# Performance work log

Measured on AMD Instinct MI355X. Metric: run time of the kernel, lower is better.

## Reference

```python
import jax, jax.numpy as jnp
import numpy as np

NUM_GROUPS = 32
EPS = 1e-5


def group_norm(x, weight, bias):
    # x: [B, C, N]
    B, C, N = x.shape
    g = x.reshape(B, NUM_GROUPS, C // NUM_GROUPS, N)
    mean = g.mean(axis=(2, 3), keepdims=True)
    var = g.var(axis=(2, 3), keepdims=True)
    g = (g - mean) * jax.lax.rsqrt(var + EPS)
    h = g.reshape(B, C, N)
    return h * weight[None, :, None] + bias[None, :, None]


def setup_inputs() -> dict:
    key = jax.random.key(0)
    ks = jax.random.split(key, 6)
    B, C, N = 2, 256, 8192
    # xavier_uniform bound for [C, C] (fan_in = fan_out = C)
    bound = float(np.sqrt(6.0 / (C + C)))
    x = jax.random.normal(ks[0], (B, C, N), dtype=jnp.float32)
    wq = jax.random.uniform(ks[1], (C, C), jnp.float32, -bound, bound)
    wk = jax.random.uniform(ks[2], (C, C), jnp.float32, -bound, bound)
    wv = jax.random.uniform(ks[3], (C, C), jnp.float32, -bound, bound)
    wp = jax.random.uniform(ks[4], (C, C), jnp.float32, -bound * 1e-5, bound * 1e-5)
    zeros = jnp.zeros((C,), jnp.float32)
    return {
        "x": x,
        "gn_weight": jnp.ones((C,), jnp.float32),
        "gn_bias": zeros,
        "wq": wq, "bq": zeros,
        "wk": wk, "bk": zeros,
        "wv": wv, "bv": zeros,
        "wp": wp, "bp": zeros,
    }


def reference(x, gn_weight, gn_bias, wq, bq, wk, bk, wv, bv, wp, bp):
    B, C, N = x.shape
    h = group_norm(x, gn_weight, gn_bias)          # [B, C, N]
    # 1x1 conv == per-position matmul over channels
    q = jnp.einsum('oc,bcn->bno', wq, h) + bq       # [B, N, C]
    k = jnp.einsum('oc,bcn->bon', wk, h) + bk[None, :, None]  # [B, C, N]
    v = jnp.einsum('oc,bcn->bno', wv, h) + bv       # [B, N, C]
    scale = C ** (-0.5)
    w = jnp.einsum('bnc,bcm->bnm', q, k) * scale    # [B, N, N]
    w = jax.nn.softmax(w, axis=-1)
    h = jnp.einsum('bnm,bmc->bnc', w, v)            # [B, N, C]
    h = jnp.einsum('oc,bnc->bon', wp, h) + bp[None, :, None]  # [B, C, N]
    return x + h
```

## Files before the change

kernel.cpp:

```cpp
#include <hip/hip_runtime.h>

#define B_ 2
#define C_ 256
#define N_ 8192
#define NG_ 32

typedef unsigned int u32;
using f32x4  = __attribute__((ext_vector_type(4))) float;
using f32x16 = __attribute__((ext_vector_type(16))) float;
using s8v    = __attribute__((ext_vector_type(8))) short;
using u32x2  = __attribute__((ext_vector_type(2))) u32;

__device__ __forceinline__ unsigned short f2bf(float f) {
  unsigned u = __builtin_bit_cast(unsigned, f);
  return (unsigned short)((u + 0x7fffu + ((u >> 16) & 1u)) >> 16);
}
__device__ __forceinline__ float bf2f(unsigned short h) {
  return __builtin_bit_cast(float, (u32)h << 16);
}
__device__ __forceinline__ u32 cvtpk(float lo, float hi) {
  u32 r;
  asm("v_cvt_pk_bf16_f32 %0, %1, %2" : "=v"(r) : "v"(lo), "v"(hi));
  return r;
}
__device__ __forceinline__ void swap32u(u32& a, u32& b) {
  asm("v_permlane32_swap_b32 %0, %1" : "+v"(a), "+v"(b));
}
__device__ __forceinline__ float xhalf_max(float x) {
  float a = x, b = x;
  asm("v_permlane32_swap_b32 %0, %1" : "+v"(a), "+v"(b));
  return fmaxf(a, b);
}
__device__ __forceinline__ float xhalf_sum(float x) {
  float a = x, b = x;
  asm("v_permlane32_swap_b32 %0, %1" : "+v"(a), "+v"(b));
  return a + b;
}

__global__ __launch_bounds__(256) void prep_kernel(
    const float* __restrict__ x,
    const float* __restrict__ wq, const float* __restrict__ wk,
    const float* __restrict__ wv, const float* __restrict__ wp,
    unsigned short* __restrict__ wout, float* __restrict__ part) {
  int t = threadIdx.x, bi = blockIdx.x;
  int j = bi * 512 + t * 2;
  int m = j >> 16;
  const float* src = m == 0 ? wq : m == 1 ? wk : m == 2 ? wv : wp;
  int off = j & 65535;
  *(u32*)(wout + j) = cvtpk(src[off], src[off + 1]);
  int bg = bi >> 3, s = bi & 7;
  const float* xp = x + (size_t)bg * 8 * N_ + s * 1024;
  float sm = 0.f, sq = 0.f;
  for (int i = t; i < 2048; i += 256) {
    int r = i >> 8, c4 = i & 255;
    f32x4 v = *(const f32x4*)(xp + (size_t)r * N_ + c4 * 4);
    sm += v.x + v.y + v.z + v.w;
    sq += v.x * v.x + v.y * v.y + v.z * v.z + v.w * v.w;
  }
  #pragma unroll
  for (int o = 32; o; o >>= 1) { sm += __shfl_down(sm, o); sq += __shfl_down(sq, o); }
  __shared__ float ls[4], lq[4];
  int w = t >> 6;
  if ((t & 63) == 0) { ls[w] = sm; lq[w] = sq; }
  __syncthreads();
  if (t == 0) {
    part[(bg * 8 + s) * 2]     = ls[0] + ls[1] + ls[2] + ls[3];
    part[(bg * 8 + s) * 2 + 1] = lq[0] + lq[1] + lq[2] + lq[3];
  }
}

__global__ __launch_bounds__(512) void qkv_kernel(
    const float* __restrict__ x, const float* __restrict__ gw, const float* __restrict__ gb,
    const float* __restrict__ part, const unsigned short* __restrict__ wqkv,
    const float* __restrict__ bq, const float* __restrict__ bk, const float* __restrict__ bv,
    unsigned short* __restrict__ Qo, unsigned short* __restrict__ Ko,
    unsigned short* __restrict__ Vo) {
  __shared__ u32 hx[256][38];
  __shared__ float gmean[32], grstd[32];
  __shared__ float scl[256], sft[256];
  const size_t HS = (size_t)N_ * C_;
  int b = blockIdx.y, n0 = blockIdx.x * 64;
  int t = threadIdx.x;

  if (t < 32) {
    float sm = 0.f, sq = 0.f;
    #pragma unroll
    for (int s = 0; s < 8; ++s) {
      sm += part[((b * 32 + t) * 8 + s) * 2];
      sq += part[((b * 32 + t) * 8 + s) * 2 + 1];
    }
    float mean = sm * (1.f / 65536.f);
    float var = sq * (1.f / 65536.f) - mean * mean;
    gmean[t] = mean;
    grstd[t] = rsqrtf(var + 1e-5f);
  }
  __syncthreads();
  if (t < 256) {
    int g = t >> 3;
    float s0 = grstd[g] * gw[t];
    scl[t] = s0;
    sft[t] = gb[t] - gmean[g] * s0;
  }
  __syncthreads();

  {
    int col2 = (t & 31) * 2;
    int c0 = t >> 5;
    const float* xb = x + (size_t)b * C_ * N_ + n0 + col2;
    #pragma unroll
    for (int r = 0; r < 16; ++r) {
      int c = r * 16 + c0;
      const float* xp = xb + (size_t)c * N_;
      float v0 = __builtin_fmaf(xp[0], scl[c], sft[c]);
      float v1 = __builtin_fmaf(xp[1], scl[c], sft[c]);
      hx[c][t & 31] = cvtpk(v0, v1);
    }
  }
  __syncthreads();

  int lane = t & 63, w = t >> 6;
  int l15 = lane & 15, lg = lane >> 4;
  int rbase = (w >> 1) * 16 + l15;
  s8v a[8];
  #pragma unroll
  for (int kt = 0; kt < 8; ++kt) {
    #pragma unroll
    for (int e = 0; e < 8; ++e) {
      u32 wd = hx[kt * 32 + lg * 8 + e][rbase >> 1];
      a[kt][e] = (short)(unsigned short)(wd >> ((rbase & 1) * 16));
    }
  }

  int gn = n0 + (w >> 1) * 16;
  int jb0 = (w & 1) * 2;
  #pragma unroll
  for (int m = 0; m < 3; ++m) {
    const unsigned short* W = wqkv + m * 65536;
    const float* bias = m == 0 ? bq : m == 1 ? bk : bv;
    #pragma unroll
    for (int jx = 0; jx < 2; ++jx) {
      int j0 = (jb0 + jx) * 64;
      f32x4 acc[4];
      #pragma unroll
      for (int jt = 0; jt < 4; ++jt) acc[jt] = f32x4{0.f, 0.f, 0.f, 0.f};
      #pragma unroll
      for (int kt = 0; kt < 8; ++kt) {
        #pragma unroll
        for (int jt = 0; jt < 4; ++jt) {
          s8v bb = *(const s8v*)(W + (size_t)(j0 + jt * 16 + l15) * 256 + kt * 32 + lg * 8);
          if (m < 2)
            acc[jt] = __builtin_amdgcn_mfma_f32_16x16x32_bf16(a[kt], bb, acc[jt], 0, 0, 0);
          else
            acc[jt] = __builtin_amdgcn_mfma_f32_16x16x32_bf16(bb, a[kt], acc[jt], 0, 0, 0);
        }
      }
      if (m < 2) {
        unsigned short* o = (m == 0 ? Qo : Ko) + (size_t)b * HS;
        int rowb = gn + lg * 4;
        #pragma unroll
        for (int jt = 0; jt < 4; ++jt) {
          int jj = j0 + jt * 16 + l15;
          float bj = bias[jj];
          #pragma unroll
          for (int r = 0; r < 4; ++r)
            o[(size_t)(rowb + r) * C_ + jj] = f2bf(acc[jt][r] + bj);
        }
      } else {
        unsigned short* o = Vo + (size_t)b * HS;
        int nn = gn + l15;
        #pragma unroll
        for (int jt = 0; jt < 4; ++jt) {
          #pragma unroll
          for (int r = 0; r < 4; ++r) {
            int oc = j0 + jt * 16 + lg * 4 + r;
            o[(size_t)oc * N_ + nn] = f2bf(acc[jt][r] + bias[oc]);
          }
        }
      }
    }
  }
}

__global__ __launch_bounds__(256) void gemm_out_kernel(
    const unsigned short* __restrict__ A,
    const unsigned short* __restrict__ Bm, long sB,
    const float* __restrict__ bias,
    const float* __restrict__ resid, long sR,
    float* __restrict__ outv, long sO, int ldo) {
  int b = blockIdx.z;
  const unsigned short* Bb = Bm + (size_t)b * sB;
  int i0 = blockIdx.x * 64, j0 = blockIdx.y * 64;
  int lane = threadIdx.x & 63, w = threadIdx.x >> 6;
  int l15 = lane & 15, lg = lane >> 4;
  const unsigned short* Ap = A + (size_t)(i0 + w * 16 + l15) * 256 + lg * 8;
  const unsigned short* Bp = Bb + (size_t)(j0 + l15) * 256 + lg * 8;
  f32x4 acc[4];
  #pragma unroll
  for (int jt = 0; jt < 4; ++jt) acc[jt] = f32x4{0.f, 0.f, 0.f, 0.f};
  #pragma unroll
  for (int kt = 0; kt < 8; ++kt) {
    s8v a = *(const s8v*)(Ap + kt * 32);
    #pragma unroll
    for (int jt = 0; jt < 4; ++jt) {
      s8v bb = *(const s8v*)(Bp + (size_t)jt * 16 * 256 + kt * 32);
      acc[jt] = __builtin_amdgcn_mfma_f32_16x16x32_bf16(a, bb, acc[jt], 0, 0, 0);
    }
  }
  int rowb = i0 + w * 16 + lg * 4;
  float* o = outv + (size_t)b * sO;
  const float* xr = resid + (size_t)b * sR;
  #pragma unroll
  for (int jt = 0; jt < 4; ++jt) {
    int j = j0 + jt * 16 + l15;
    #pragma unroll
    for (int r = 0; r < 4; ++r) {
      size_t idx = (size_t)(rowb + r) * ldo + j;
      o[idx] = acc[jt][r] + bias[rowb + r] + xr[idx];
    }
  }
}

__global__ __launch_bounds__(256, 2) void attn_kernel(
    const unsigned short* __restrict__ Q, const unsigned short* __restrict__ K,
    const unsigned short* __restrict__ V, unsigned short* __restrict__ Op,
    float* __restrict__ lse) {
  extern __shared__ unsigned short smem[];
  int f = blockIdx.x;
  int grp = f & 7, qb = f >> 3;
  int sl = grp & 3, b = grp >> 2;
  int q0 = qb * 128;
  int kvbase = sl * 2048;
  int t = threadIdx.x, lane = t & 63, w = t >> 6;
  int l31 = lane & 31, hi = lane >> 5;

  const unsigned short* Qg = Q + ((size_t)b * N_ + q0 + w * 32 + l31) * 256;
  const unsigned short* Kg = K + ((size_t)b * N_ + kvbase) * 256;
  const unsigned short* Vg = V + (size_t)b * 256 * N_ + kvbase;
  const float sc = 0.0625f * 1.44269504088896f;

  s8v qf[16];
  #pragma unroll
  for (int tt = 0; tt < 16; ++tt)
    qf[tt] = *(const s8v*)(Qg + tt * 16 + hi * 8);

  f32x16 o_acc[8];
  #pragma unroll
  for (int dc = 0; dc < 8; ++dc)
    #pragma unroll
    for (int r = 0; r < 16; ++r) o_acc[dc][r] = 0.f;
  float m_r = -1e30f, l_r = 0.f;

  auto stage = [&](int it, int bufsel) {
    char* Kd = (char*)smem + bufsel * 16384;
    char* Vd = (char*)smem + 32768 + bufsel * 16384;
    const unsigned short* Ks = Kg + (size_t)it * 32 * 256;
    const unsigned short* Vs = Vg + it * 32;
    #pragma unroll
    for (int i = 0; i < 4; ++i) {
      int u = i * 256 + t;
      int mm = u >> 5, j = u & 31;
      const unsigned short* src = Ks + mm * 256 + ((j ^ mm) * 8);
      char* dst = Kd + (i * 256 + w * 64) * 16;
      __builtin_amdgcn_global_load_lds(
          (const __attribute__((address_space(1))) u32*)src,
          (__attribute__((address_space(3))) u32*)dst, 16, 0, 0);
    }
    #pragma unroll
    for (int i = 0; i < 4; ++i) {
      const unsigned short* src = Vs + (size_t)t * N_ + i * 8;
      char* dst = Vd + (i * 256 + w * 64) * 16;
      __builtin_amdgcn_global_load_lds(
          (const __attribute__((address_space(1))) u32*)src,
          (__attribute__((address_space(3))) u32*)dst, 16, 0, 0);
    }
  };

  stage(0, 0);
  __syncthreads();

  for (int it = 0; it < 64; ++it) {
    int cur = it & 1;
    if (it + 1 < 64) stage(it + 1, cur ^ 1);
    const char* Kd = (const char*)smem + cur * 16384;
    const char* Vd = (const char*)smem + 32768 + cur * 16384;

    f32x16 sa;
    #pragma unroll
    for (int r = 0; r < 16; ++r) sa[r] = 0.f;
    __builtin_amdgcn_s_setprio(1);
    #pragma unroll
    for (int tt = 0; tt < 16; ++tt) {
      int slot = 2 * tt + hi;
      s8v ka = *(const s8v*)(Kd + l31 * 512 + ((slot ^ l31) * 16));
      sa = __builtin_amdgcn_mfma_f32_32x32x16_bf16(ka, qf[tt], sa, 0, 0, 0);
    }
    __builtin_amdgcn_s_setprio(0);

    float rmax = sa[0];
    #pragma unroll
    for (int r = 1; r < 16; ++r) rmax = fmaxf(rmax, sa[r]);
    rmax = xhalf_max(rmax);
    rmax *= sc;
    if (!__all(rmax <= m_r + 8.f)) {
      float mn = fmaxf(m_r, rmax);
      float corr = exp2f(m_r - mn);
      m_r = mn;
      l_r *= corr;
      #pragma unroll
      for (int dc = 0; dc < 8; ++dc)
        #pragma unroll
        for (int r = 0; r < 16; ++r) o_acc[dc][r] *= corr;
    }
    float rs = 0.f;
    u32 wv[8];
    #pragma unroll
    for (int j = 0; j < 8; ++j) {
      float p0 = exp2f(__builtin_fmaf(sa[2 * j],     sc, -m_r));
      float p1 = exp2f(__builtin_fmaf(sa[2 * j + 1], sc, -m_r));
      rs += p0 + p1;
      wv[j] = cvtpk(p0, p1);
    }
    l_r += xhalf_sum(rs);

    swap32u(wv[0], wv[2]);
    swap32u(wv[1], wv[3]);
    swap32u(wv[4], wv[6]);
    swap32u(wv[5], wv[7]);
    union { u32 u[4]; s8v v; } pf0, pf1;
    pf0.u[0] = wv[0]; pf0.u[1] = wv[1]; pf0.u[2] = wv[2]; pf0.u[3] = wv[3];
    pf1.u[0] = wv[4]; pf1.u[1] = wv[5]; pf1.u[2] = wv[6]; pf1.u[3] = wv[7];

    __builtin_amdgcn_s_setprio(1);
    #pragma unroll
    for (int dc = 0; dc < 8; ++dc) {
      s8v va0 = *(const s8v*)(Vd + ((hi) * 256 + dc * 32 + l31) * 16);
      o_acc[dc] = __builtin_amdgcn_mfma_f32_32x32x16_bf16(va0, pf0.v, o_acc[dc], 0, 0, 0);
      s8v va1 = *(const s8v*)(Vd + ((2 + hi) * 256 + dc * 32 + l31) * 16);
      o_acc[dc] = __builtin_amdgcn_mfma_f32_32x32x16_bf16(va1, pf1.v, o_acc[dc], 0, 0, 0);
    }
    __builtin_amdgcn_s_setprio(0);
    __syncthreads();
  }

  float inv = 1.f / l_r;
  size_t rid = (size_t)b * N_ + q0 + w * 32 + l31;
  if (!hi) lse[(size_t)sl * (B_ * N_) + rid] = m_r + log2f(l_r);
  unsigned short* Od = Op + ((size_t)sl * (B_ * N_) + rid) * 256;
  #pragma unroll
  for (int dc = 0; dc < 8; ++dc) {
    #pragma unroll
    for (int rg = 0; rg < 4; ++rg) {
      int d0 = dc * 32 + 8 * rg + 4 * hi;
      u32 w0 = cvtpk(o_acc[dc][rg * 4 + 0] * inv, o_acc[dc][rg * 4 + 1] * inv);
      u32 w1 = cvtpk(o_acc[dc][rg * 4 + 2] * inv, o_acc[dc][rg * 4 + 3] * inv);
      u32x2 pk{w0, w1};
      *(u32x2*)(Od + d0) = pk;
    }
  }
}

__global__ __launch_bounds__(256) void attn_merge_kernel(
    const unsigned short* __restrict__ Op, const float* __restrict__ lse,
    unsigned short* __restrict__ Ob) {
  int gid = blockIdx.x * 256 + threadIdx.x;
  int row = gid >> 5;
  int co = (gid & 31) * 8;
  float L[4], lm = -1e30f;
  #pragma unroll
  for (int s = 0; s < 4; ++s) { L[s] = lse[s * (B_ * N_) + row]; lm = fmaxf(lm, L[s]); }
  float acc[8];
  #pragma unroll
  for (int e = 0; e < 8; ++e) acc[e] = 0.f;
  float wsum = 0.f;
  #pragma unroll
  for (int s = 0; s < 4; ++s) {
    float wg = exp2f(L[s] - lm);
    wsum += wg;
    s8v v = *(const s8v*)(Op + ((size_t)s * (B_ * N_) + row) * 256 + co);
    #pragma unroll
    for (int e = 0; e < 8; ++e) acc[e] += wg * bf2f((unsigned short)v[e]);
  }
  float inv = 1.f / wsum;
  s8v o;
  #pragma unroll
  for (int e = 0; e < 8; ++e) o[e] = (short)f2bf(acc[e] * inv);
  *(s8v*)(Ob + (size_t)row * 256 + co) = o;
}

extern "C" void kernel_launch(void* const* d_in, const int* in_sizes, int n_in,
                              void* d_out, int out_size, void* d_ws, size_t ws_size,
                              hipStream_t stream) {
  (void)in_sizes; (void)n_in; (void)out_size; (void)ws_size;
  const float* x  = (const float*)d_in[0];
  const float* gw = (const float*)d_in[1];
  const float* gb = (const float*)d_in[2];
  const float* wq = (const float*)d_in[3];
  const float* bq = (const float*)d_in[4];
  const float* wk = (const float*)d_in[5];
  const float* bk = (const float*)d_in[6];
  const float* wv = (const float*)d_in[7];
  const float* bv = (const float*)d_in[8];
  const float* wp = (const float*)d_in[9];
  const float* bp = (const float*)d_in[10];

  const size_t HS = (size_t)N_ * C_;
  char* ws = (char*)d_ws;
  unsigned short* wqb = (unsigned short*)ws;
  float* part = (float*)(ws + 524288);
  unsigned short* Qb   = (unsigned short*)(ws + 528384);
  unsigned short* Kb   = Qb + B_ * HS;
  unsigned short* Vb   = Kb + B_ * HS;
  unsigned short* Ob   = Vb + B_ * HS;
  unsigned short* Opart = Ob + B_ * HS;
  float* lsep = (float*)(Opart + 4 * B_ * HS);

  prep_kernel<<<512, 256, 0, stream>>>(x, wq, wk, wv, wp, wqb, part);

  qkv_kernel<<<dim3(N_ / 64, B_), 512, 0, stream>>>(
      x, gw, gb, part, wqb, bq, bk, bv, Qb, Kb, Vb);

  const int attn_lds = 65536;
  hipFuncSetAttribute(reinterpret_cast<const void*>(attn_kernel),
                      hipFuncAttributeMaxDynamicSharedMemorySize, attn_lds);
  attn_kernel<<<dim3(512), 256, attn_lds, stream>>>(Qb, Kb, Vb, Opart, lsep);

  attn_merge_kernel<<<(B_ * N_ * 32) / 256, 256, 0, stream>>>(Opart, lsep, Ob);

  unsigned short* wpb = wqb + 3 * 65536;
  gemm_out_kernel<<<dim3(C_ / 64, N_ / 64, B_), 256, 0, stream>>>(
      wpb, Ob, (long)HS, bp, x, (long)HS, (float*)d_out, (long)HS, N_);
}
```

Measured before the change: 240.9 us.

## Fuse split-KV attention merge into output projection GEMM via LDS staging

Replaces the separate merge kernel and output projection GEMM with one kernel. Each block merges four partial attention outputs for 32 rows using LSE weights, stages the bf16 result in swizzled shared memory, then runs the Wp projection with MFMA and adds bias and the residual. This drops a kernel launch and the global write and re-read of the merged O buffer. In exchange each block reloads all of Wp from global/L2 and works on a small 32-row tile, which may lower MFMA efficiency.

```diff
diff --git a/kernel.cpp b/kernel.cpp
--- a/kernel.cpp
+++ b/kernel.cpp
@@ -181,45 +181,6 @@
   }
 }
 
-__global__ __launch_bounds__(256) void gemm_out_kernel(
-    const unsigned short* __restrict__ A,
-    const unsigned short* __restrict__ Bm, long sB,
-    const float* __restrict__ bias,
-    const float* __restrict__ resid, long sR,
-    float* __restrict__ outv, long sO, int ldo) {
-  int b = blockIdx.z;
-  const unsigned short* Bb = Bm + (size_t)b * sB;
-  int i0 = blockIdx.x * 64, j0 = blockIdx.y * 64;
-  int lane = threadIdx.x & 63, w = threadIdx.x >> 6;
-  int l15 = lane & 15, lg = lane >> 4;
-  const unsigned short* Ap = A + (size_t)(i0 + w * 16 + l15) * 256 + lg * 8;
-  const unsigned short* Bp = Bb + (size_t)(j0 + l15) * 256 + lg * 8;
-  f32x4 acc[4];
-  #pragma unroll
-  for (int jt = 0; jt < 4; ++jt) acc[jt] = f32x4{0.f, 0.f, 0.f, 0.f};
-  #pragma unroll
-  for (int kt = 0; kt < 8; ++kt) {
-    s8v a = *(const s8v*)(Ap + kt * 32);
-    #pragma unroll
-    for (int jt = 0; jt < 4; ++jt) {
-      s8v bb = *(const s8v*)(Bp + (size_t)jt * 16 * 256 + kt * 32);
-      acc[jt] = __builtin_amdgcn_mfma_f32_16x16x32_bf16(a, bb, acc[jt], 0, 0, 0);
-    }
-  }
-  int rowb = i0 + w * 16 + lg * 4;
-  float* o = outv + (size_t)b * sO;
-  const float* xr = resid + (size_t)b * sR;
-  #pragma unroll
-  for (int jt = 0; jt < 4; ++jt) {
-    int j = j0 + jt * 16 + l15;
-    #pragma unroll
-    for (int r = 0; r < 4; ++r) {
-      size_t idx = (size_t)(rowb + r) * ldo + j;
-      o[idx] = acc[jt][r] + bias[rowb + r] + xr[idx];
-    }
-  }
-}
-
 __global__ __launch_bounds__(256, 2) void attn_kernel(
     const unsigned short* __restrict__ Q, const unsigned short* __restrict__ K,
     const unsigned short* __restrict__ V, unsigned short* __restrict__ Op,
@@ -359,32 +320,88 @@
   }
 }
 
-__global__ __launch_bounds__(256) void attn_merge_kernel(
+__global__ __launch_bounds__(256) void out_kernel(
     const unsigned short* __restrict__ Op, const float* __restrict__ lse,
-    unsigned short* __restrict__ Ob) {
-  int gid = blockIdx.x * 256 + threadIdx.x;
-  int row = gid >> 5;
-  int co = (gid & 31) * 8;
+    const unsigned short* __restrict__ W, const float* __restrict__ bias,
+    const float* __restrict__ x, float* __restrict__ out) {
+  __shared__ unsigned short hx[32][32][8];
+  int b = blockIdx.y, n0 = blockIdx.x * 32;
+  int t = threadIdx.x;
+
+  int row = t >> 3;
+  int ch8 = t & 7;
+  size_t rid = (size_t)b * N_ + n0 + row;
   float L[4], lm = -1e30f;
   #pragma unroll
-  for (int s = 0; s < 4; ++s) { L[s] = lse[s * (B_ * N_) + row]; lm = fmaxf(lm, L[s]); }
-  float acc[8];
-  #pragma unroll
-  for (int e = 0; e < 8; ++e) acc[e] = 0.f;
-  float wsum = 0.f;
-  #pragma unroll
   for (int s = 0; s < 4; ++s) {
-    float wg = exp2f(L[s] - lm);
-    wsum += wg;
-    s8v v = *(const s8v*)(Op + ((size_t)s * (B_ * N_) + row) * 256 + co);
-    #pragma unroll
-    for (int e = 0; e < 8; ++e) acc[e] += wg * bf2f((unsigned short)v[e]);
-  }
+    L[s] = lse[(size_t)s * (B_ * N_) + rid];
+    lm = fmaxf(lm, L[s]);
+  }
+  float wg[4], wsum = 0.f;
+  #pragma unroll
+  for (int s = 0; s < 4; ++s) { wg[s] = exp2f(L[s] - lm); wsum += wg[s]; }
   float inv = 1.f / wsum;
-  s8v o;
-  #pragma unroll
-  for (int e = 0; e < 8; ++e) o[e] = (short)f2bf(acc[e] * inv);
-  *(s8v*)(Ob + (size_t)row * 256 + co) = o;
+  #pragma unroll
+  for (int s = 0; s < 4; ++s) wg[s] *= inv;
+  #pragma unroll
+  for (int cb = 0; cb < 4; ++cb) {
+    int chunk = cb * 8 + ch8;
+    float acc[8];
+    #pragma unroll
+    for (int e = 0; e < 8; ++e) acc[e] = 0.f;
+    #pragma unroll
+    for (int s = 0; s < 4; ++s) {
+      s8v v = *(const s8v*)(Op + ((size_t)s * (B_ * N_) + rid) * 256 + chunk * 8);
+      #pragma unroll
+      for (int e = 0; e < 8; ++e)
+        acc[e] = __builtin_fmaf(wg[s], bf2f((unsigned short)v[e]), acc[e]);
+    }
+    union { u32 u[4]; s8v v; } pk;
+    pk.u[0] = cvtpk(acc[0], acc[1]);
+    pk.u[1] = cvtpk(acc[2], acc[3]);
+    pk.u[2] = cvtpk(acc[4], acc[5]);
+    pk.u[3] = cvtpk(acc[6], acc[7]);
+    *(s8v*)&hx[row][chunk ^ row][0] = pk.v;
+  }
+  __syncthreads();
+
+  int lane = t & 63, w = t >> 6;
+  int l15 = lane & 15, lg = lane >> 4;
+  f32x4 acc[4][2];
+  #pragma unroll
+  for (int ct = 0; ct < 4; ++ct)
+    #pragma unroll
+    for (int jt = 0; jt < 2; ++jt) acc[ct][jt] = f32x4{0.f, 0.f, 0.f, 0.f};
+  #pragma unroll
+  for (int kt = 0; kt < 8; ++kt) {
+    s8v bb[2];
+    #pragma unroll
+    for (int jt = 0; jt < 2; ++jt) {
+      int n = jt * 16 + l15;
+      bb[jt] = *(const s8v*)&hx[n][(kt * 4 + lg) ^ n][0];
+    }
+    #pragma unroll
+    for (int ct = 0; ct < 4; ++ct) {
+      s8v aa = *(const s8v*)(W + (size_t)(w * 64 + ct * 16 + l15) * 256 + kt * 32 + lg * 8);
+      #pragma unroll
+      for (int jt = 0; jt < 2; ++jt)
+        acc[ct][jt] = __builtin_amdgcn_mfma_f32_16x16x32_bf16(aa, bb[jt], acc[ct][jt], 0, 0, 0);
+    }
+  }
+  #pragma unroll
+  for (int ct = 0; ct < 4; ++ct) {
+    #pragma unroll
+    for (int r = 0; r < 4; ++r) {
+      int c = w * 64 + ct * 16 + lg * 4 + r;
+      float bc = bias[c];
+      size_t base = ((size_t)b * C_ + c) * N_ + n0;
+      #pragma unroll
+      for (int jt = 0; jt < 2; ++jt) {
+        int n = jt * 16 + l15;
+        out[base + n] = acc[ct][jt][r] + bc + x[base + n];
+      }
+    }
+  }
 }
 
 extern "C" void kernel_launch(void* const* d_in, const int* in_sizes, int n_in,
@@ -410,8 +427,7 @@
   unsigned short* Qb   = (unsigned short*)(ws + 528384);
   unsigned short* Kb   = Qb + B_ * HS;
   unsigned short* Vb   = Kb + B_ * HS;
-  unsigned short* Ob   = Vb + B_ * HS;
-  unsigned short* Opart = Ob + B_ * HS;
+  unsigned short* Opart = Vb + B_ * HS;
   float* lsep = (float*)(Opart + 4 * B_ * HS);
 
   prep_kernel<<<512, 256, 0, stream>>>(x, wq, wk, wv, wp, wqb, part);
@@ -424,9 +440,7 @@
                       hipFuncAttributeMaxDynamicSharedMemorySize, attn_lds);
   attn_kernel<<<dim3(512), 256, attn_lds, stream>>>(Qb, Kb, Vb, Opart, lsep);
 
-  attn_merge_kernel<<<(B_ * N_ * 32) / 256, 256, 0, stream>>>(Opart, lsep, Ob);
-
   unsigned short* wpb = wqb + 3 * 65536;
-  gemm_out_kernel<<<dim3(C_ / 64, N_ / 64, B_), 256, 0, stream>>>(
-      wpb, Ob, (long)HS, bp, x, (long)HS, (float*)d_out, (long)HS, N_);
-}
+  out_kernel<<<dim3(N_ / 32, B_), 256, 0, stream>>>(
+      Opart, lsep, wpb, bp, x, (float*)d_out);
+}
```

Result: faster. 228.9 us (-5.0%).
